# Performance work log

Hardware: AMD Instinct MI355X
Metric: run time of the kernel (lower is better)

The kernel has to match this reference:

```python
import jax, jax.numpy as jnp
import numpy as np

VIS = 1024
HID = 1024
DIM = VIS + HID
INIT_ITERS = 1000   # init_gibbs_iters
KL_SAMPLES = 10     # kl_gibbs_samples
TOTAL_STEPS = INIT_ITERS + INIT_ITERS + KL_SAMPLES  # warm-up + (clip + k) loop = 2010
BETA = 1.0
TEMP = 0.2
N = 8192


def setup_inputs() -> dict:
    key = jax.random.key(0)
    ks = jax.random.split(key, 8)
    vecs = jax.random.normal(ks[0], (N, 2 * 1024), jnp.float32)
    logits_w = jax.random.normal(ks[1], (2 * 1024, DIM), jnp.float32) * 0.02
    logits_b = jnp.zeros((DIM,), jnp.float32)
    w = jax.random.normal(ks[2], (VIS, HID), jnp.float32)
    bv = jnp.zeros((1, VIS), jnp.float32)
    bh = jnp.zeros((1, HID), jnp.float32)
    # logistic reparametrization noise: log(U/(1-U))
    u = jax.random.uniform(ks[3], (N, DIM), jnp.float32, 1e-6, 1.0 - 1e-6)
    epsilon = jnp.log(u / (1.0 - u))
    u_init = jax.random.uniform(ks[4], (1, VIS), jnp.float32)
    u_h = jax.random.uniform(ks[5], (TOTAL_STEPS, 1, HID), jnp.float32)
    u_v = jax.random.uniform(ks[6], (TOTAL_STEPS, 1, VIS), jnp.float32)
    return {"vecs": vecs, "logits_w": logits_w, "logits_b": logits_b, "w": w,
            "bv": bv, "bh": bh, "epsilon": epsilon, "u_init": u_init,
            "u_h": u_h, "u_v": u_v}


def _bern(u, p):
    # sample_bernoulli: where(rand - p < 0, 0, 1)  -> 1 iff u >= p
    return (u >= p).astype(p.dtype)


def _run_gibbs(w, bv, bh, u_init, u_h, u_v):
    def step(sv, us):
        uh, uv = us
        sh = _bern(uh, jax.nn.sigmoid(bh + sv @ w))         # propup + sample
        sv2 = _bern(uv, jax.nn.sigmoid(bv + sh @ w.T))      # propdown + sample
        return sv2, (sv2, sh)

    sv0 = _bern(u_init, jnp.full((1, VIS), 0.5, u_init.dtype))
    # warm-up: init_gibbs_iters steps, keep only final visible state
    sv1, _ = jax.lax.scan(step, sv0, (u_h[:INIT_ITERS], u_v[:INIT_ITERS]))
    # sampling loop: clip + k steps; only the last KL_SAMPLES are kept
    _, (svs, shs) = jax.lax.scan(step, sv1, (u_h[INIT_ITERS:], u_v[INIT_ITERS:]))
    samples = jnp.concatenate(
        [svs[-KL_SAMPLES:, 0], shs[-KL_SAMPLES:, 0]], axis=1)  # [KL_SAMPLES, DIM]
    return samples


def reference(vecs, logits_w, logits_b, w, bv, bh, epsilon, u_init, u_h, u_v):
    logits = vecs @ logits_w + logits_b                     # [N, DIM]
    zeta = jax.nn.sigmoid((logits + epsilon) / TEMP)        # inverse_reparametrize

    samples = _run_gibbs(w, bv, bh, u_init, u_h, u_v)       # [KL_SAMPLES, DIM]

    b = jnp.concatenate([bv, bh], axis=1)                   # [1, DIM]

    def free_energy(s):
        sv_, sh_ = s[:, :VIS], s[:, VIS:]
        return jnp.sum(s * b, axis=1) + jnp.sum((sv_ @ w) * sh_, axis=1)

    probs = jax.nn.sigmoid(logits)
    log_posterior = jnp.sum(
        jnp.log(zeta * probs + (1.0 - zeta) * (1.0 - probs)), axis=-1)
    log_prior_un = -free_energy(zeta)
    kl = jnp.mean(log_posterior - log_prior_un) - jnp.mean(free_energy(samples))
    kl = BETA * kl
    return zeta[:, :VIS], zeta[:, VIS:], kl
```

## Files before the change

kernel.cpp:

```cpp
#include <hip/hip_runtime.h>
#include <math.h>

#define VIS 1024
#define HID 1024
#define NROW 8192
#define KDIM 2048
#define NDIM 2048
#define NSTEPS 2010
#define KLS 10

__global__ __launch_bounds__(256) void init_zero(float* p, int n) {
    int i = blockIdx.x * 256 + threadIdx.x;
    if (i < n) p[i] = 0.f;
}

__global__ __launch_bounds__(256) void transpose_w_k(const float* __restrict__ w,
                                                     float* __restrict__ wT) {
    __shared__ float tile[32][33];
    int bx = blockIdx.x * 32, by = blockIdx.y * 32;
    int tx = threadIdx.x & 31, ty = threadIdx.x >> 5;
    #pragma unroll
    for (int m = 0; m < 4; ++m) {
        int y = by + ty + m * 8;
        tile[ty + m * 8][tx] = w[(size_t)y * 1024 + bx + tx];
    }
    __syncthreads();
    #pragma unroll
    for (int m = 0; m < 4; ++m) {
        int y = bx + ty + m * 8;
        wT[(size_t)y * 1024 + by + tx] = tile[tx][ty + m * 8];
    }
}

__global__ __launch_bounds__(256) void prep_thr(
    const float* __restrict__ u_h, const float* __restrict__ u_v,
    const float* __restrict__ bh, const float* __restrict__ bv,
    double* __restrict__ thrH, double* __restrict__ thrV)
{
    int i = blockIdx.x * 256 + threadIdx.x;
    if (i < NSTEPS * 1024) {
        int jj = i & 1023;
        double uh = (double)u_h[i];
        thrH[i] = log(uh) - log1p(-uh) - (double)bh[jj];
        double uv = (double)u_v[i];
        thrV[i] = log(uv) - log1p(-uv) - (double)bv[jj];
    }
}

struct SGibbs {
    int wcnt[16] __attribute__((aligned(16)));
    int sidx[1040] __attribute__((aligned(16)));
    double redd[4];
};
struct SMm1 {
    float As[8][128];
    float Bs[8][128];
    float red[128 * 17];
};
union SharedU { SGibbs g; SMm1 m; };

__device__ __forceinline__ int build4(SGibbs& sg, const bool* fl, const bool* nb,
                                      int t, int wv, int lane, int tid) {
    unsigned long long m[4];
    #pragma unroll
    for (int k = 0; k < 4; ++k) m[k] = __ballot(fl[k]);
    if (lane == 0) {
        #pragma unroll
        for (int k = 0; k < 4; ++k) sg.wcnt[wv * 4 + k] = __popcll(m[k]);
    }
    __syncthreads();
    const int4* wc = (const int4*)sg.wcnt;
    int4 c0 = wc[0], c1 = wc[1], c2 = wc[2], c3 = wc[3];
    int cs[16] = {c0.x, c0.y, c0.z, c0.w, c1.x, c1.y, c1.z, c1.w,
                  c2.x, c2.y, c2.z, c2.w, c3.x, c3.y, c3.z, c3.w};
    int n = 0, offk[4] = {0, 0, 0, 0};
    const int base4 = wv * 4;
    #pragma unroll
    for (int u = 0; u < 16; ++u) {
        int cu = cs[u];
        #pragma unroll
        for (int k = 0; k < 4; ++k) offk[k] += (u < base4 + k) ? cu : 0;
        n += cu;
    }
    unsigned long long below = (1ull << lane) - 1ull;
    #pragma unroll
    for (int k = 0; k < 4; ++k)
        if (fl[k])
            sg.sidx[offk[k] + __popcll(m[k] & below)] =
                (((4 * t + k)) << 12) | 2 | (nb[k] ? 1 : 0);
    int npad = (n + 7) & ~7;
    if (tid < npad - n) sg.sidx[n + tid] = 0;
    __syncthreads();
    return npad;
}

#define LOADE(base, e, v)                                                  \
    {                                                                      \
        int4 _a = *(const int4*)&sg.sidx[(base)];                          \
        int4 _b = *(const int4*)&sg.sidx[(base) + 4];                      \
        e[0] = _a.x; e[1] = _a.y; e[2] = _a.z; e[3] = _a.w;                \
        e[4] = _b.x; e[5] = _b.y; e[6] = _b.z; e[7] = _b.w;                \
        _Pragma("unroll")                                                  \
        for (int _q = 0; _q < 8; ++_q)                                     \
            v[_q] = *(const float4*)(Mb + (e[_q] & 0x3FF000));             \
    }
#define PROC(e, v)                                                         \
    {                                                                      \
        _Pragma("unroll")                                                  \
        for (int _q = 0; _q < 8; ++_q) {                                   \
            double _s = (e[_q] & 2) ? ((e[_q] & 1) ? 1.0 : -1.0) : 0.0;    \
            dot[0] = fma(_s, (double)v[_q].x, dot[0]);                     \
            dot[1] = fma(_s, (double)v[_q].y, dot[1]);                     \
            dot[2] = fma(_s, (double)v[_q].z, dot[2]);                     \
            dot[3] = fma(_s, (double)v[_q].w, dot[3]);                     \
        }                                                                  \
    }

__device__ __forceinline__ void apply_ph(double* dot, const SGibbs& sg, int npad,
                                         const char* Mb) {
    int eA[8], eB[8];
    float4 vA[8], vB[8];
    LOADE(0, eA, vA);
    for (int i = 8; i < npad; i += 8) {
        LOADE(i, eB, vB);
        PROC(eA, vA);
        #pragma unroll
        for (int q = 0; q < 8; ++q) { eA[q] = eB[q]; vA[q] = vB[q]; }
    }
    PROC(eA, vA);
}

__global__ __launch_bounds__(256) void fused_k(
    const float* __restrict__ w, const float* __restrict__ wT,
    const float* __restrict__ bv, const float* __restrict__ bh,
    const float* __restrict__ u_init, const float* __restrict__ u_h,
    const float* __restrict__ u_v, double* __restrict__ fes,
    const double* __restrict__ thrHp, const double* __restrict__ thrVp, int use_pre,
    const float* __restrict__ A, const float* __restrict__ B,
    const float* __restrict__ lb, const float* __restrict__ eps,
    float* __restrict__ zv, float* __restrict__ zh, float* __restrict__ lp_row)
{
    __shared__ SharedU su;
    const int tid = threadIdx.x;

    if (blockIdx.x == 0) {
        SGibbs& sg = su.g;
        const int t4 = tid;
        const int wv = tid >> 6, lane = tid & 63;
        const char* wjb  = (const char*)w  + (size_t)t4 * 16;
        const char* wTjb = (const char*)wT + (size_t)t4 * 16;
        double doth[4] = {0, 0, 0, 0}, dotv[4] = {0, 0, 0, 0};
        double fe_acc = 0.0;

        bool mv[4], mh[4] = {false, false, false, false};
        {
            float4 ui = *(const float4*)&u_init[4 * t4];
            mv[0] = ui.x >= 0.5f; mv[1] = ui.y >= 0.5f;
            mv[2] = ui.z >= 0.5f; mv[3] = ui.w >= 0.5f;
        }
        double thH[4], thV[4];
        #pragma unroll
        for (int k = 0; k < 4; ++k) {
            if (use_pre) { thH[k] = thrHp[4 * t4 + k]; thV[k] = thrVp[4 * t4 + k]; }
            else {
                double uh = (double)u_h[4 * t4 + k];
                thH[k] = log(uh) - log1p(-uh) - (double)bh[4 * t4 + k];
                double uv = (double)u_v[4 * t4 + k];
                thV[k] = log(uv) - log1p(-uv) - (double)bv[4 * t4 + k];
            }
        }
        {
            bool nb1[4] = {true, true, true, true};
            int np0 = build4(sg, mv, nb1, t4, wv, lane, tid);
            { double* dot = doth; const char* Mb = wjb; apply_ph(dot, sg, np0, Mb); }
        }

        for (int t = 0; t < NSTEPS; ++t) {
            bool nh[4], flH[4];
            #pragma unroll
            for (int k = 0; k < 4; ++k) { nh[k] = (doth[k] <= thH[k]); flH[k] = (nh[k] != mh[k]); mh[k] = nh[k]; }
            double thHn[4];
            if (t + 1 < NSTEPS) {
                if (use_pre) {
                    double2 a = *(const double2*)&thrHp[(size_t)(t + 1) * 1024 + 4 * t4];
                    double2 b = *(const double2*)&thrHp[(size_t)(t + 1) * 1024 + 4 * t4 + 2];
                    thHn[0] = a.x; thHn[1] = a.y; thHn[2] = b.x; thHn[3] = b.y;
                } else {
                    #pragma unroll
                    for (int k = 0; k < 4; ++k) {
                        double u = (double)u_h[(size_t)(t + 1) * 1024 + 4 * t4 + k];
                        thHn[k] = log(u) - log1p(-u) - (double)bh[4 * t4 + k];
                    }
                }
            }
            int np = build4(sg, flH, nh, t4, wv, lane, tid);
            { double* dot = dotv; const char* Mb = wTjb; apply_ph(dot, sg, np, Mb); }

            bool nv[4], flV[4];
            #pragma unroll
            for (int k = 0; k < 4; ++k) { nv[k] = (dotv[k] <= thV[k]); flV[k] = (nv[k] != mv[k]); mv[k] = nv[k]; }
            if (t + 1 < NSTEPS) {
                if (use_pre) {
                    double2 a = *(const double2*)&thrVp[(size_t)(t + 1) * 1024 + 4 * t4];
                    double2 b = *(const double2*)&thrVp[(size_t)(t + 1) * 1024 + 4 * t4 + 2];
                    thV[0] = a.x; thV[1] = a.y; thV[2] = b.x; thV[3] = b.y;
                } else {
                    #pragma unroll
                    for (int k = 0; k < 4; ++k) {
                        double u = (double)u_v[(size_t)(t + 1) * 1024 + 4 * t4 + k];
                        thV[k] = log(u) - log1p(-u) - (double)bv[4 * t4 + k];
                    }
                }
                #pragma unroll
                for (int k = 0; k < 4; ++k) thH[k] = thHn[k];
            }
            np = build4(sg, flV, nv, t4, wv, lane, tid);
            { double* dot = doth; const char* Mb = wjb; apply_ph(dot, sg, np, Mb); }

            if (t >= NSTEPS - KLS) {
                double c = 0.0;
                #pragma unroll
                for (int k = 0; k < 4; ++k) {
                    double bvk = (double)bv[4 * t4 + k], bhk = (double)bh[4 * t4 + k];
                    c += (nv[k] ? bvk : 0.0) + (nh[k] ? (bhk + doth[k]) : 0.0);
                }
                #pragma unroll
                for (int o = 32; o > 0; o >>= 1) c += __shfl_down(c, o);
                if (lane == 0) sg.redd[wv] = c;
                __syncthreads();
                if (tid == 0)
                    fe_acc += sg.redd[0] + sg.redd[1] + sg.redd[2] + sg.redd[3];
                __syncthreads();
            }
        }
        if (tid == 0) fes[0] = fe_acc;
        return;
    }

    const int gid = blockIdx.x - 1;
    const int n0 = (gid & 15) * 128;
    const int m0 = (gid >> 4) * 128;
    const int tx = tid & 15, ty = tid >> 4;
    const int ar = tid >> 1, ac = (tid & 1) * 4;
    const int br = tid >> 5, bc = (tid & 31) * 4;

    float acc[8][8];
    #pragma unroll
    for (int i = 0; i < 8; ++i)
        #pragma unroll
        for (int j = 0; j < 8; ++j) acc[i][j] = 0.f;

    float4 a_reg = *reinterpret_cast<const float4*>(&A[(size_t)(m0 + ar) * KDIM + ac]);
    float4 b_reg = *reinterpret_cast<const float4*>(&B[(size_t)br * NDIM + n0 + bc]);
    for (int k0 = 0; k0 < KDIM; k0 += 8) {
        __syncthreads();
        su.m.As[ac + 0][ar] = a_reg.x; su.m.As[ac + 1][ar] = a_reg.y;
        su.m.As[ac + 2][ar] = a_reg.z; su.m.As[ac + 3][ar] = a_reg.w;
        *reinterpret_cast<float4*>(&su.m.Bs[br][bc]) = b_reg;
        __syncthreads();
        if (k0 + 8 < KDIM) {
            a_reg = *reinterpret_cast<const float4*>(&A[(size_t)(m0 + ar) * KDIM + k0 + 8 + ac]);
            b_reg = *reinterpret_cast<const float4*>(&B[(size_t)(k0 + 8 + br) * NDIM + n0 + bc]);
        }
        #pragma unroll
        for (int k = 0; k < 8; ++k) {
            float av[8], bw[8];
            const float4* ap = reinterpret_cast<const float4*>(&su.m.As[k][ty * 8]);
            const float4* bp = reinterpret_cast<const float4*>(&su.m.Bs[k][tx * 8]);
            float4 a0 = ap[0], a1 = ap[1], b0 = bp[0], b1 = bp[1];
            av[0]=a0.x; av[1]=a0.y; av[2]=a0.z; av[3]=a0.w; av[4]=a1.x; av[5]=a1.y; av[6]=a1.z; av[7]=a1.w;
            bw[0]=b0.x; bw[1]=b0.y; bw[2]=b0.z; bw[3]=b0.w; bw[4]=b1.x; bw[5]=b1.y; bw[6]=b1.z; bw[7]=b1.w;
            #pragma unroll
            for (int i = 0; i < 8; ++i)
                #pragma unroll
                for (int j = 0; j < 8; ++j)
                    acc[i][j] = fmaf(av[i], bw[j], acc[i][j]);
        }
    }

    const bool isv = (n0 < VIS);
    float lpacc[8];
    #pragma unroll
    for (int i = 0; i < 8; ++i) {
        const int row = m0 + ty * 8 + i;
        float s = 0.f;
        #pragma unroll
        for (int j = 0; j < 8; ++j) {
            const int n = n0 + tx * 8 + j;
            float l = acc[i][j] + lb[n];
            float e = eps[(size_t)row * NDIM + n];
            float z = 1.f / (1.f + expf(-(l + e) * 5.f));
            float p = 1.f / (1.f + expf(-l));
            float bb;
            if (isv) { zv[(size_t)row * VIS + n] = z; bb = bv[n]; }
            else     { zh[(size_t)row * HID + (n - VIS)] = z; bb = bh[n - VIS]; }
            s += logf(z * p + (1.f - z) * (1.f - p)) + z * bb;
        }
        lpacc[i] = s;
    }
    __syncthreads();
    #pragma unroll
    for (int i = 0; i < 8; ++i) su.m.red[(ty * 8 + i) * 17 + tx] = lpacc[i];
    __syncthreads();
    if (tid < 128) {
        float s = 0.f;
        #pragma unroll
        for (int x = 0; x < 16; ++x) s += su.m.red[tid * 17 + x];
        atomicAdd(&lp_row[m0 + tid], s);
    }
}

#define BM 128
#define BN 128
#define BK 8

__global__ __launch_bounds__(256) void gemm2_fe(
    const float* __restrict__ A, const float* __restrict__ B,
    const float* __restrict__ ZH, float* __restrict__ fe_row)
{
    __shared__ float As[BK][BM];
    __shared__ float Bs[BK][BN];
    __shared__ float red[BM * 17];
    const int tid = threadIdx.x;
    const int n0 = blockIdx.x * BN;
    const int m0 = blockIdx.y * BM;
    const int tx = tid & 15, ty = tid >> 4;
    const int ar = tid >> 1, ac = (tid & 1) * 4;
    const int br = tid >> 5, bc = (tid & 31) * 4;

    float acc[8][8];
    #pragma unroll
    for (int i = 0; i < 8; ++i)
        #pragma unroll
        for (int j = 0; j < 8; ++j) acc[i][j] = 0.f;

    for (int k0 = 0; k0 < 1024; k0 += BK) {
        float4 a = *reinterpret_cast<const float4*>(&A[(size_t)(m0 + ar) * 1024 + k0 + ac]);
        float4 b = *reinterpret_cast<const float4*>(&B[(size_t)(k0 + br) * 1024 + n0 + bc]);
        __syncthreads();
        As[ac + 0][ar] = a.x; As[ac + 1][ar] = a.y; As[ac + 2][ar] = a.z; As[ac + 3][ar] = a.w;
        *reinterpret_cast<float4*>(&Bs[br][bc]) = b;
        __syncthreads();
        #pragma unroll
        for (int k = 0; k < BK; ++k) {
            float av[8], bw[8];
            const float4* ap = reinterpret_cast<const float4*>(&As[k][ty * 8]);
            const float4* bp = reinterpret_cast<const float4*>(&Bs[k][tx * 8]);
            float4 a0 = ap[0], a1 = ap[1], b0 = bp[0], b1 = bp[1];
            av[0]=a0.x; av[1]=a0.y; av[2]=a0.z; av[3]=a0.w; av[4]=a1.x; av[5]=a1.y; av[6]=a1.z; av[7]=a1.w;
            bw[0]=b0.x; bw[1]=b0.y; bw[2]=b0.z; bw[3]=b0.w; bw[4]=b1.x; bw[5]=b1.y; bw[6]=b1.z; bw[7]=b1.w;
            #pragma unroll
            for (int i = 0; i < 8; ++i)
                #pragma unroll
                for (int j = 0; j < 8; ++j)
                    acc[i][j] = fmaf(av[i], bw[j], acc[i][j]);
        }
    }

    float feacc[8];
    #pragma unroll
    for (int i = 0; i < 8; ++i) {
        const int row = m0 + ty * 8 + i;
        float s = 0.f;
        #pragma unroll
        for (int j = 0; j < 8; ++j) {
            const int n = n0 + tx * 8 + j;
            s += acc[i][j] * ZH[(size_t)row * HID + n];
        }
        feacc[i] = s;
    }
    __syncthreads();
    #pragma unroll
    for (int i = 0; i < 8; ++i) red[(ty * 8 + i) * 17 + tx] = feacc[i];
    __syncthreads();
    if (tid < BM) {
        float s = 0.f;
        #pragma unroll
        for (int x = 0; x < 16; ++x) s += red[tid * 17 + x];
        atomicAdd(&fe_row[m0 + tid], s);
    }
}

__global__ __launch_bounds__(256) void final_kl(
    const float* __restrict__ lp_row, const float* __restrict__ fe_row,
    const double* __restrict__ fe_sum, float* __restrict__ out_kl)
{
    __shared__ double dred[256];
    const int tid = threadIdx.x;
    double acc = 0.0;
    for (int r = tid; r < NROW; r += 256)
        acc += (double)lp_row[r] + (double)fe_row[r];
    dred[tid] = acc;
    __syncthreads();
    for (int off = 128; off > 0; off >>= 1) {
        if (tid < off) dred[tid] += dred[tid + off];
        __syncthreads();
    }
    if (tid == 0) out_kl[0] = (float)(dred[0] / 8192.0 - fe_sum[0] / 10.0);
}

extern "C" void kernel_launch(void* const* d_in, const int* in_sizes, int n_in,
                              void* d_out, int out_size, void* d_ws, size_t ws_size,
                              hipStream_t stream)
{
    const float* vecs   = (const float*)d_in[0];
    const float* lw     = (const float*)d_in[1];
    const float* lb     = (const float*)d_in[2];
    const float* w      = (const float*)d_in[3];
    const float* bv     = (const float*)d_in[4];
    const float* bh     = (const float*)d_in[5];
    const float* eps    = (const float*)d_in[6];
    const float* u_init = (const float*)d_in[7];
    const float* u_h    = (const float*)d_in[8];
    const float* u_v    = (const float*)d_in[9];

    float* out    = (float*)d_out;
    float* zv     = out;
    float* zh     = out + (size_t)NROW * VIS;
    float* out_kl = out + (size_t)NROW * 2048;

    const size_t thr_sz = (size_t)NSTEPS * 1024 * 8;
    const size_t pre_need = (4u << 20) + 2 * thr_sz + 65536 + 64;
    const int use_pre = (ws_size >= pre_need) ? 1 : 0;

    char* ws = (char*)d_ws;
    float*  wT   = (float*)ws;
    double* thrH = use_pre ? (double*)(ws + (4u << 20)) : nullptr;
    double* thrV = use_pre ? (double*)(ws + (4u << 20) + thr_sz) : nullptr;
    size_t tail  = (4u << 20) + (use_pre ? 2 * thr_sz : 0);
    float*  lp_row = (float*)(ws + tail);
    float*  fe_row = lp_row + 8192;
    double* fes    = (double*)(ws + tail + 65536);

    init_zero<<<64, 256, 0, stream>>>(lp_row, 16384);
    transpose_w_k<<<dim3(32, 32), 256, 0, stream>>>(w, wT);
    if (use_pre)
        prep_thr<<<(NSTEPS * 1024 + 255) / 256, 256, 0, stream>>>(u_h, u_v, bh, bv, thrH, thrV);
    fused_k<<<1 + 1024, 256, 0, stream>>>(
        w, wT, bv, bh, u_init, u_h, u_v, fes, thrH, thrV, use_pre,
        vecs, lw, lb, eps, zv, zh, lp_row);
    gemm2_fe<<<dim3(8, 64), 256, 0, stream>>>(zv, w, zh, fe_row);
    final_kl<<<1, 256, 0, stream>>>(lp_row, fe_row, fes, out_kl);
}
```

Baseline: 5.213 ms.

## Simplify flip-list compaction, deepen gather prefetch, and overlap threshold loads in Gibbs loop

The compaction of flipped units is rewritten to use one count per wavefront and a contiguous per-thread layout. This replaces the 16-entry prefix computation with a 4-entry one. The sparse weight-row gather in apply_ph now keeps two chunks of 8 rows in flight instead of one, to hide more memory latency in the single-block serial Gibbs chain. The next-step threshold loads are issued after the list build so they overlap with the gather. Accumulation order of the double-precision dots changes, and register pressure goes up.

```diff
diff --git a/kernel.cpp b/kernel.cpp
--- a/kernel.cpp
+++ b/kernel.cpp
@@ -48,7 +48,7 @@
 }
 
 struct SGibbs {
-    int wcnt[16] __attribute__((aligned(16)));
+    int wcnt[4] __attribute__((aligned(16)));
     int sidx[1040] __attribute__((aligned(16)));
     double redd[4];
 };
@@ -60,34 +60,23 @@
 union SharedU { SGibbs g; SMm1 m; };
 
 __device__ __forceinline__ int build4(SGibbs& sg, const bool* fl, const bool* nb,
-                                      int t, int wv, int lane, int tid) {
-    unsigned long long m[4];
-    #pragma unroll
-    for (int k = 0; k < 4; ++k) m[k] = __ballot(fl[k]);
-    if (lane == 0) {
-        #pragma unroll
-        for (int k = 0; k < 4; ++k) sg.wcnt[wv * 4 + k] = __popcll(m[k]);
-    }
-    __syncthreads();
-    const int4* wc = (const int4*)sg.wcnt;
-    int4 c0 = wc[0], c1 = wc[1], c2 = wc[2], c3 = wc[3];
-    int cs[16] = {c0.x, c0.y, c0.z, c0.w, c1.x, c1.y, c1.z, c1.w,
-                  c2.x, c2.y, c2.z, c2.w, c3.x, c3.y, c3.z, c3.w};
-    int n = 0, offk[4] = {0, 0, 0, 0};
-    const int base4 = wv * 4;
-    #pragma unroll
-    for (int u = 0; u < 16; ++u) {
-        int cu = cs[u];
-        #pragma unroll
-        for (int k = 0; k < 4; ++k) offk[k] += (u < base4 + k) ? cu : 0;
-        n += cu;
-    }
+                                      int wv, int lane, int tid) {
+    unsigned long long m0 = __ballot(fl[0]), m1 = __ballot(fl[1]),
+                       m2 = __ballot(fl[2]), m3 = __ballot(fl[3]);
+    if (lane == 0)
+        sg.wcnt[wv] = __popcll(m0) + __popcll(m1) + __popcll(m2) + __popcll(m3);
+    __syncthreads();
+    int c0 = sg.wcnt[0], c1 = sg.wcnt[1], c2 = sg.wcnt[2], c3 = sg.wcnt[3];
+    int n = c0 + c1 + c2 + c3;
+    int off = (wv > 0 ? c0 : 0) + (wv > 1 ? c1 : 0) + (wv > 2 ? c2 : 0);
     unsigned long long below = (1ull << lane) - 1ull;
-    #pragma unroll
-    for (int k = 0; k < 4; ++k)
-        if (fl[k])
-            sg.sidx[offk[k] + __popcll(m[k] & below)] =
-                (((4 * t + k)) << 12) | 2 | (nb[k] ? 1 : 0);
+    int base = off + __popcll(m0 & below) + __popcll(m1 & below)
+                   + __popcll(m2 & below) + __popcll(m3 & below);
+    const int r0 = tid << 2;
+    if (fl[0]) sg.sidx[base++] = ((r0    ) << 12) | 2 | (nb[0] ? 1 : 0);
+    if (fl[1]) sg.sidx[base++] = ((r0 + 1) << 12) | 2 | (nb[1] ? 1 : 0);
+    if (fl[2]) sg.sidx[base++] = ((r0 + 2) << 12) | 2 | (nb[2] ? 1 : 0);
+    if (fl[3]) sg.sidx[base++] = ((r0 + 3) << 12) | 2 | (nb[3] ? 1 : 0);
     int npad = (n + 7) & ~7;
     if (tid < npad - n) sg.sidx[n + tid] = 0;
     __syncthreads();
@@ -118,16 +107,22 @@
 
 __device__ __forceinline__ void apply_ph(double* dot, const SGibbs& sg, int npad,
                                          const char* Mb) {
-    int eA[8], eB[8];
-    float4 vA[8], vB[8];
-    LOADE(0, eA, vA);
-    for (int i = 8; i < npad; i += 8) {
-        LOADE(i, eB, vB);
-        PROC(eA, vA);
-        #pragma unroll
-        for (int q = 0; q < 8; ++q) { eA[q] = eB[q]; vA[q] = vB[q]; }
-    }
-    PROC(eA, vA);
+    int nch = npad >> 3;
+    if (nch == 0) return;
+    int e0[8], e1[8], e2[8];
+    float4 v0[8], v1[8], v2[8];
+    LOADE(0, e0, v0);
+    if (nch > 1) LOADE(8, e1, v1);
+    int c = 0;
+    for (; c + 3 < nch; c += 2) {
+        PROC(e0, v0); LOADE((c + 2) * 8, e0, v0);
+        PROC(e1, v1); LOADE((c + 3) * 8, e1, v1);
+    }
+    int rem = nch - c;
+    if (rem == 3) LOADE((c + 2) * 8, e2, v2);
+    PROC(e0, v0);
+    if (rem >= 2) PROC(e1, v1);
+    if (rem == 3) PROC(e2, v2);
 }
 
 __global__ __launch_bounds__(256) void fused_k(
@@ -171,7 +166,7 @@
         }
         {
             bool nb1[4] = {true, true, true, true};
-            int np0 = build4(sg, mv, nb1, t4, wv, lane, tid);
+            int np0 = build4(sg, mv, nb1, wv, lane, tid);
             { double* dot = doth; const char* Mb = wjb; apply_ph(dot, sg, np0, Mb); }
         }
 
@@ -179,7 +174,8 @@
             bool nh[4], flH[4];
             #pragma unroll
             for (int k = 0; k < 4; ++k) { nh[k] = (doth[k] <= thH[k]); flH[k] = (nh[k] != mh[k]); mh[k] = nh[k]; }
-            double thHn[4];
+            int np = build4(sg, flH, nh, wv, lane, tid);
+            double thHn[4] = {0, 0, 0, 0};
             if (t + 1 < NSTEPS) {
                 if (use_pre) {
                     double2 a = *(const double2*)&thrHp[(size_t)(t + 1) * 1024 + 4 * t4];
@@ -193,29 +189,32 @@
                     }
                 }
             }
-            int np = build4(sg, flH, nh, t4, wv, lane, tid);
             { double* dot = dotv; const char* Mb = wTjb; apply_ph(dot, sg, np, Mb); }
 
             bool nv[4], flV[4];
             #pragma unroll
             for (int k = 0; k < 4; ++k) { nv[k] = (dotv[k] <= thV[k]); flV[k] = (nv[k] != mv[k]); mv[k] = nv[k]; }
+            np = build4(sg, flV, nv, wv, lane, tid);
+            double thVn[4] = {0, 0, 0, 0};
             if (t + 1 < NSTEPS) {
                 if (use_pre) {
                     double2 a = *(const double2*)&thrVp[(size_t)(t + 1) * 1024 + 4 * t4];
                     double2 b = *(const double2*)&thrVp[(size_t)(t + 1) * 1024 + 4 * t4 + 2];
-                    thV[0] = a.x; thV[1] = a.y; thV[2] = b.x; thV[3] = b.y;
+                    thVn[0] = a.x; thVn[1] = a.y; thVn[2] = b.x; thVn[3] = b.y;
                 } else {
                     #pragma unroll
                     for (int k = 0; k < 4; ++k) {
                         double u = (double)u_v[(size_t)(t + 1) * 1024 + 4 * t4 + k];
-                        thV[k] = log(u) - log1p(-u) - (double)bv[4 * t4 + k];
+                        thVn[k] = log(u) - log1p(-u) - (double)bv[4 * t4 + k];
                     }
                 }
+            }
+            { double* dot = doth; const char* Mb = wjb; apply_ph(dot, sg, np, Mb); }
+
+            if (t + 1 < NSTEPS) {
                 #pragma unroll
-                for (int k = 0; k < 4; ++k) thH[k] = thHn[k];
+                for (int k = 0; k < 4; ++k) { thH[k] = thHn[k]; thV[k] = thVn[k]; }
             }
-            np = build4(sg, flV, nv, t4, wv, lane, tid);
-            { double* dot = doth; const char* Mb = wjb; apply_ph(dot, sg, np, Mb); }
 
             if (t >= NSTEPS - KLS) {
                 double c = 0.0;
```

After: 4.425 ms. 15.1% less time.
